# Kernel optimization log

Hardware: AMD Instinct MI355X
Metric: run time of the kernel (lower is better)

## Reference

```python
import jax, jax.numpy as jnp
import numpy as np

N_NODES = 50000


def _degree_norms(edge_index, n_nodes):
    # PyG GCNConv: add self-loops, deg = 1 + in-degree at target (col)
    src, dst = edge_index[0], edge_index[1]
    deg = 1.0 + jax.ops.segment_sum(jnp.ones(src.shape[0], jnp.float32), dst,
                                    num_segments=n_nodes)
    d_inv_sqrt = 1.0 / jnp.sqrt(deg)  # deg >= 1 always (self-loop)
    norm_e = d_inv_sqrt[src] * d_inv_sqrt[dst]   # per-edge sym norm
    norm_self = d_inv_sqrt * d_inv_sqrt          # self-loop weight
    return norm_e, norm_self


def _gcn_conv(x, W, b, src, dst, norm_e, norm_self, n_nodes):
    h = x @ W                                    # [N, F_out]
    msg = h[src] * norm_e[:, None]               # gather + scale, [E, F_out]
    agg = jax.ops.segment_sum(msg, dst, num_segments=n_nodes)
    return agg + norm_self[:, None] * h + b


def setup_inputs() -> dict:
    key = jax.random.key(0)
    ks = jax.random.split(key, 10)
    F_in, H = 128, 128
    E = 1_600_000
    x = jax.random.normal(ks[0], (N_NODES, F_in), jnp.float32)
    edge_index = jax.random.randint(ks[1], (2, E), 0, N_NODES, dtype=jnp.int64)

    def glorot(k, fi, fo):
        s = jnp.sqrt(6.0 / (fi + fo)).astype(jnp.float32)
        return jax.random.uniform(k, (fi, fo), jnp.float32, -s, s)

    return {
        "x": x,
        "edge_index": edge_index,
        "W1": glorot(ks[2], F_in, H), "b1": jnp.zeros((H,), jnp.float32),
        "W2": glorot(ks[3], H, H),    "b2": jnp.zeros((H,), jnp.float32),
        "W3": glorot(ks[4], H, H),    "b3": jnp.zeros((H,), jnp.float32),
        "W4": glorot(ks[5], H, 1),    "b4": jnp.zeros((1,), jnp.float32),
    }


def reference(x, edge_index, W1, b1, W2, b2, W3, b3, W4, b4):
    src, dst = edge_index[0], edge_index[1]
    norm_e, norm_self = _degree_norms(edge_index, N_NODES)
    h = jax.nn.relu(_gcn_conv(x, W1, b1, src, dst, norm_e, norm_self, N_NODES))
    h = jax.nn.relu(_gcn_conv(h, W2, b2, src, dst, norm_e, norm_self, N_NODES))
    h = jax.nn.relu(_gcn_conv(h, W3, b3, src, dst, norm_e, norm_self, N_NODES))
    return _gcn_conv(h, W4, b4, src, dst, norm_e, norm_self, N_NODES)
```

## Files before the change

### kernel.cpp

```cpp
#include <hip/hip_runtime.h>
#include <hip/hip_bf16.h>
#include <stdint.h>

typedef unsigned int u32;
typedef unsigned short u16;

#define F 128
#define NBUCK 196
#define SLOTS 9216

typedef __attribute__((ext_vector_type(8))) short bf16x8;
typedef __attribute__((ext_vector_type(8))) u16 u16x8;
typedef __attribute__((ext_vector_type(4))) float f32x4;

__device__ __forceinline__ float bf2f(u16 v){
  union { u32 u; float f; } x; x.u = ((u32)v) << 16; return x.f;
}
__device__ __forceinline__ float bflo(u32 w){
  union { u32 u; float f; } x; x.u = w << 16; return x.f;
}
__device__ __forceinline__ float bfhi(u32 w){
  union { u32 u; float f; } x; x.u = w & 0xFFFF0000u; return x.f;
}
__device__ __forceinline__ u16 f2bf(float f){
  union { float f; u32 u; } x; x.f = f;
  u32 u = x.u;
  return (u16)((u + 0x7fffu + ((u >> 16) & 1u)) >> 16);
}
__device__ __forceinline__ bf16x8 as_bf(u16x8 v){
  union { u16x8 a; bf16x8 b; } u; u.a = v; return u.b;
}
__device__ __forceinline__ int detect_f32(const u32* xw){
  u32 hit = 0;
  for (int i = threadIdx.x; i < 2048; i += 256){
    u32 e = (xw[i] >> 7) & 0xFFu;
    if (e > 160u) hit = 1;
  }
  return __syncthreads_or((int)hit);
}
__device__ __forceinline__ int detect_stride(const u32* ei){
  u32 v = 0;
  for (int i = threadIdx.x; i < 4096; i += 256) v |= ei[2*i + 1];
  return __syncthreads_or((int)v) ? 1 : 2;
}

__global__ void k_setup(const void* x0,
                        const void* b1, const void* b2, const void* b3,
                        const void* W1, const void* W2, const void* W3,
                        const void* W4, const void* b4,
                        float* __restrict__ bb, float* __restrict__ wf4,
                        float* __restrict__ bb4, u16* __restrict__ WL,
                        int* __restrict__ bump){
  int t = threadIdx.x, b = blockIdx.x;
  int f32 = detect_f32((const u32*)x0);
  if (b == 0){
    bump[t] = 0;
    for (int i = t; i < 384; i += 256){
      const void* s = (i < 128) ? b1 : ((i < 256) ? b2 : b3);
      int ii = i & 127;
      bb[i] = f32 ? ((const float*)s)[ii] : bf2f(((const u16*)s)[ii]);
    }
    if (t < 128) wf4[t] = f32 ? ((const float*)W4)[t] : bf2f(((const u16*)W4)[t]);
    if (t == 0)  bb4[0] = f32 ? ((const float*)b4)[0] : bf2f(((const u16*)b4)[0]);
  } else {
    int bb_ = b - 1;
    int l = bb_ >> 6;
    const void* W = (l == 0) ? W1 : ((l == 1) ? W2 : W3);
    int idx = (bb_ & 63)*256 + t;
    int j    = idx & 7;
    int lane = (idx >> 3) & 63;
    int kb   = (idx >> 9) & 3;
    int ct   = idx >> 11;
    int m = lane & 15, q = lane >> 4;
    int k = kb*32 + q*8 + j;
    int c = ct*16 + m;
    float v = f32 ? ((const float*)W)[k*F + c] : bf2f(((const u16*)W)[k*F + c]);
    WL[l*16384 + idx] = f2bf(v);
  }
}

__launch_bounds__(256)
__global__ void k_msplit(const u32* __restrict__ w, int E,
                         int* __restrict__ bump, u32* __restrict__ ebuf){
  __shared__ int h[256];
  __shared__ int cb[256];
  int st = detect_stride(w);
  int t = threadIdx.x;
  h[t] = 0;
  __syncthreads();
  int base = blockIdx.x*4096;
  u32 ps[16]; int bk[16]; int rk[16];
  #pragma unroll 4
  for (int k = 0; k < 16; k++){
    int i = base + k*256 + t;
    if (i < E){
      u32 s = w[(size_t)i*st];
      u32 d = w[(size_t)(E + i)*st];
      bk[k] = (int)(d >> 8);
      ps[k] = (s & 0xFFFFu) | ((d & 0xFFu) << 16);
      rk[k] = atomicAdd(&h[bk[k]], 1);
    } else bk[k] = -1;
  }
  __syncthreads();
  cb[t] = h[t] ? (t*SLOTS + atomicAdd(&bump[t], h[t])) : 0;
  __syncthreads();
  #pragma unroll 4
  for (int k = 0; k < 16; k++){
    if (bk[k] >= 0) ebuf[cb[bk[k]] + rk[k]] = ps[k];
  }
}

__launch_bounds__(256)
__global__ void k_bemit(const u32* __restrict__ ebuf, const int* __restrict__ bump,
                        int N, int* __restrict__ deg, int* __restrict__ rs,
                        u16* __restrict__ csr, float* __restrict__ dis){
  __shared__ int nd[256];
  __shared__ int nofs[256];
  __shared__ int s[256];
  int b = blockIdx.x;
  int t = threadIdx.x;
  int e0 = b*SLOTS, e1 = e0 + bump[b];
  nd[t] = 0;
  __syncthreads();
  for (int i = e0 + t; i < e1; i += 256) atomicAdd(&nd[ebuf[i] >> 16], 1);
  __syncthreads();
  int v = nd[t];
  s[t] = v;
  __syncthreads();
  for (int off = 1; off < 256; off <<= 1){
    int x = (t >= off) ? s[t - off] : 0;
    __syncthreads();
    s[t] += x;
    __syncthreads();
  }
  nofs[t] = s[t] - v;
  int node = b*256 + t;
  if (node < N){
    deg[node] = v;
    rs[node]  = e0 + nofs[t];
    dis[node] = rsqrtf(1.0f + (float)v);
  }
  nd[t] = 0;
  __syncthreads();
  for (int i = e0 + t; i < e1; i += 256){
    u32 p = ebuf[i];
    int d = (int)(p >> 16);
    int pos = e0 + nofs[d] + atomicAdd(&nd[d], 1);
    csr[pos] = (u16)(p & 0xFFFFu);
  }
}

__launch_bounds__(256)
__global__ void k_mm(const u16* __restrict__ X, const void* __restrict__ Xraw,
                     const u16* __restrict__ WL, const float* __restrict__ dis,
                     u16* __restrict__ G, int N, int mode){
  int f32 = 0;
  if (mode) f32 = detect_f32((const u32*)Xraw);
  int w = threadIdx.x >> 6, lane = threadIdx.x & 63;
  int m = lane & 15, q = lane >> 4;
  int row0 = blockIdx.x*64 + w*16;
  int arow = row0 + m;
  u16x8 a[4];
  if (arow < N){
    if (mode == 0){
      const u16* xp = X + (size_t)arow*F;
      #pragma unroll
      for (int kb = 0; kb < 4; kb++) a[kb] = *(const u16x8*)(xp + kb*32 + q*8);
    } else if (f32){
      const float* xp = (const float*)Xraw + (size_t)arow*F;
      #pragma unroll
      for (int kb = 0; kb < 4; kb++){
        f32x4 v0 = *(const f32x4*)(xp + kb*32 + q*8);
        f32x4 v1 = *(const f32x4*)(xp + kb*32 + q*8 + 4);
        u16x8 o;
        #pragma unroll
        for (int k = 0; k < 4; k++){ o[k] = f2bf(v0[k]); o[k+4] = f2bf(v1[k]); }
        a[kb] = o;
      }
    } else {
      const u16* xp = (const u16*)Xraw + (size_t)arow*F;
      #pragma unroll
      for (int kb = 0; kb < 4; kb++) a[kb] = *(const u16x8*)(xp + kb*32 + q*8);
    }
  } else {
    #pragma unroll
    for (int kb = 0; kb < 4; kb++) a[kb] = (u16x8){0,0,0,0,0,0,0,0};
  }
  f32x4 acc[8];
  #pragma unroll
  for (int ct = 0; ct < 8; ct++) acc[ct] = (f32x4){0.f,0.f,0.f,0.f};
  #pragma unroll
  for (int ct = 0; ct < 8; ct++){
    #pragma unroll
    for (int kb = 0; kb < 4; kb++){
      bf16x8 bfr = *(const bf16x8*)(WL + ((size_t)((ct*4 + kb)*64 + lane))*8);
      acc[ct] = __builtin_amdgcn_mfma_f32_16x16x32_bf16(as_bf(a[kb]), bfr, acc[ct], 0, 0, 0);
    }
  }
  int rbase = row0 + q*4;
  #pragma unroll
  for (int r = 0; r < 4; r++){
    int row = rbase + r;
    if (row < N){
      float dv = dis[row];
      #pragma unroll
      for (int ct = 0; ct < 8; ct++)
        __builtin_nontemporal_store(f2bf(dv*acc[ct][r]),
                                    &G[(size_t)row*F + ct*16 + m]);
    }
  }
}

__launch_bounds__(256)
__global__ void k_agg(const u16* __restrict__ G, const float* __restrict__ dis,
                      const int* __restrict__ rs, const int* __restrict__ deg,
                      const u16* __restrict__ csr, const float* __restrict__ bias,
                      u16* __restrict__ Xout, const float* __restrict__ W4f,
                      float* __restrict__ G4, int N, int fuse4){
  int wid  = blockIdx.x*4 + (threadIdx.x >> 6);
  int lane = threadIdx.x & 63;
  if (wid >= N) return;
  int base = rs[wid], len = deg[wid];
  const char* Gb = (const char*)G;
  u32 fo = 4u*(u32)lane;
  u32 sw = *(const u32*)(Gb + (((size_t)(u32)wid) << 8) + fo);
  float a0 = bflo(sw), a1 = bfhi(sw);
  float pa[8], qa[8];
  #pragma unroll
  for (int k = 0; k < 8; k++){ pa[k] = 0.f; qa[k] = 0.f; }

  int mm = (len < 64) ? len : 64;
  u32 soff = ((u32)csr[base + lane]) << 8;
  int c0 = 0;
  while (c0 < len){
    int nxt = c0 + 64;
    int nmm = len - nxt; if (nmm > 64) nmm = 64;
    u32 soff_n = 0;
    if (nmm > 0) soff_n = ((u32)csr[base + nxt + lane]) << 8;
    int j = 0;
    for (; j + 8 <= mm; j += 8){
      u32 w[8];
      #pragma unroll
      for (int k = 0; k < 8; k++){
        u32 o = (u32)__builtin_amdgcn_readlane((int)soff, j + k);
        w[k] = *(const u32*)(Gb + o + fo);
      }
      #pragma unroll
      for (int k = 0; k < 8; k++){
        pa[k] += bflo(w[k]); qa[k] += bfhi(w[k]);
      }
    }
    for (; j < mm; j++){
      u32 o = (u32)__builtin_amdgcn_readlane((int)soff, j);
      u32 wv = *(const u32*)(Gb + o + fo);
      pa[0] += bflo(wv); qa[0] += bfhi(wv);
    }
    soff = soff_n; mm = nmm; c0 = nxt;
  }
  a0 += ((pa[0] + pa[1]) + (pa[2] + pa[3])) + ((pa[4] + pa[5]) + (pa[6] + pa[7]));
  a1 += ((qa[0] + qa[1]) + (qa[2] + qa[3])) + ((qa[4] + qa[5]) + (qa[6] + qa[7]));
  float dv = dis[wid];
  float o0 = fmaxf(fmaf(dv, a0, bias[2*lane]),     0.f);
  float o1 = fmaxf(fmaf(dv, a1, bias[2*lane + 1]), 0.f);
  if (!fuse4){
    u32 pk = (u32)f2bf(o0) | ((u32)f2bf(o1) << 16);
    __builtin_nontemporal_store(pk, (u32*)(Xout + (size_t)wid*F + 2*lane));
  } else {
    float acc = o0*W4f[2*lane] + o1*W4f[2*lane + 1];
    #pragma unroll
    for (int off = 32; off > 0; off >>= 1) acc += __shfl_down(acc, off, 64);
    if (lane == 0) G4[wid] = dv*acc;
  }
}

__global__ void k_agg4(const void* __restrict__ x0, const float* __restrict__ G4,
                       const float* __restrict__ dis, const int* __restrict__ rs,
                       const int* __restrict__ deg, const u16* __restrict__ csr,
                       const float* __restrict__ b4f, void* __restrict__ out, int N){
  int f32 = detect_f32((const u32*)x0);
  int i = blockIdx.x*blockDim.x + threadIdx.x;
  if (i >= N) return;
  int base = rs[i], len = deg[i];
  float a0 = 0.f, a1 = 0.f, a2 = 0.f, a3 = 0.f;
  int j = 0;
  for (; j + 4 <= len; j += 4){
    int s0 = csr[base + j],     s1 = csr[base + j + 1];
    int s2 = csr[base + j + 2], s3 = csr[base + j + 3];
    a0 += G4[s0]; a1 += G4[s1]; a2 += G4[s2]; a3 += G4[s3];
  }
  for (; j < len; j++) a0 += G4[csr[base + j]];
  float r = dis[i]*(G4[i] + ((a0 + a1) + (a2 + a3))) + b4f[0];
  if (f32) ((float*)out)[i] = r;
  else     ((u16*)out)[i]   = f2bf(r);
}

extern "C" void kernel_launch(void* const* d_in, const int* in_sizes, int n_in,
                              void* d_out, int out_size, void* d_ws, size_t ws_size,
                              hipStream_t stream){
  const void* x0 = d_in[0];
  const u32*  ei = (const u32*)d_in[1];
  const void* Wp[4] = {d_in[2], d_in[4], d_in[6], d_in[8]};
  const void* bp[4] = {d_in[3], d_in[5], d_in[7], d_in[9]};
  int N = in_sizes[0] / F;
  int E = in_sizes[1] / 2;

  char* base = (char*)d_ws;
  size_t off = 0;
  auto alloc = [&](size_t bytes)->char*{
    char* p = base + off;
    off = (off + bytes + 255) & ~(size_t)255;
    return p;
  };
  int*   deg  = (int*)  alloc((size_t)N*4);
  float* dis  = (float*)alloc((size_t)N*4);
  int*   rs   = (int*)  alloc((size_t)N*4);
  float* g4   = (float*)alloc((size_t)N*4);
  int*   bump = (int*)  alloc(1024);
  u32*   ebuf = (u32*)  alloc(((size_t)NBUCK*SLOTS + 64)*4);
  u16*   csr  = (u16*)  alloc(((size_t)NBUCK*SLOTS + 128)*2);
  u16*   WL   = (u16*)  alloc(3*16384*2);
  float* wf4  = (float*)alloc(F*4);
  float* bb   = (float*)alloc(3*F*4);
  float* bb4  = (float*)alloc(256);
  u16*   gbuf = (u16*)  alloc((size_t)N*F*2);
  u16*   xbuf = (u16*)  alloc((size_t)N*F*2);

  int etb = (E + 4095)/4096;
  int nbt = (N + 255)/256;

  k_setup<<<193, 256, 0, stream>>>(x0, bp[0], bp[1], bp[2],
                                   Wp[0], Wp[1], Wp[2], Wp[3], bp[3],
                                   bb, wf4, bb4, WL, bump);
  k_msplit<<<etb, 256, 0, stream>>>(ei, E, bump, ebuf);
  k_bemit <<<NBUCK, 256, 0, stream>>>(ebuf, bump, N, deg, rs, csr, dis);

  int mmb = (N + 63)/64;
  int agb = (N + 3)/4;

  for (int l = 0; l < 3; l++){
    k_mm <<<mmb, 256, 0, stream>>>(xbuf, (l == 0) ? x0 : (const void*)xbuf,
                                   WL + l*16384, dis, gbuf, N, (l == 0) ? 1 : 0);
    k_agg<<<agb, 256, 0, stream>>>(gbuf, dis, rs, deg, csr, bb + l*F, xbuf,
                                   wf4, g4, N, (l == 2) ? 1 : 0);
  }
  k_agg4<<<nbt, 256, 0, stream>>>(x0, g4, dis, rs, deg, csr, bb4, (void*)d_out, N);
}
```

Before: 345.6 us.

## Transpose MFMA output for packed row stores and use wave-per-node final aggregation

The matmul kernel swaps the MFMA operands so each lane holds four consecutive output columns of a single row. It can then pack them into 8-byte stores instead of scattering 2-byte stores across rows. The final scalar aggregation kernel changes from thread-per-node to wave-per-node with a shuffle reduction, which spreads the gather over lanes and removes per-thread load imbalance. The price is more launched waves and reduction overhead in the last layer.

```diff
diff --git a/kernel.cpp b/kernel.cpp
--- a/kernel.cpp
+++ b/kernel.cpp
@@ -12,6 +12,7 @@
 typedef __attribute__((ext_vector_type(8))) short bf16x8;
 typedef __attribute__((ext_vector_type(8))) u16 u16x8;
 typedef __attribute__((ext_vector_type(4))) float f32x4;
+typedef __attribute__((ext_vector_type(2))) u32 u32x2;
 
 __device__ __forceinline__ float bf2f(u16 v){
   union { u32 u; float f; } x; x.u = ((u32)v) << 16; return x.f;
@@ -194,19 +195,18 @@
     #pragma unroll
     for (int kb = 0; kb < 4; kb++){
       bf16x8 bfr = *(const bf16x8*)(WL + ((size_t)((ct*4 + kb)*64 + lane))*8);
-      acc[ct] = __builtin_amdgcn_mfma_f32_16x16x32_bf16(as_bf(a[kb]), bfr, acc[ct], 0, 0, 0);
-    }
-  }
-  int rbase = row0 + q*4;
-  #pragma unroll
-  for (int r = 0; r < 4; r++){
-    int row = rbase + r;
-    if (row < N){
-      float dv = dis[row];
-      #pragma unroll
-      for (int ct = 0; ct < 8; ct++)
-        __builtin_nontemporal_store(f2bf(dv*acc[ct][r]),
-                                    &G[(size_t)row*F + ct*16 + m]);
+      acc[ct] = __builtin_amdgcn_mfma_f32_16x16x32_bf16(bfr, as_bf(a[kb]), acc[ct], 0, 0, 0);
+    }
+  }
+  if (arow < N){
+    float dv = dis[arow];
+    u16* gp = G + (size_t)arow*F + q*4;
+    #pragma unroll
+    for (int ct = 0; ct < 8; ct++){
+      u32x2 pk;
+      pk.x = (u32)f2bf(dv*acc[ct][0]) | ((u32)f2bf(dv*acc[ct][1]) << 16);
+      pk.y = (u32)f2bf(dv*acc[ct][2]) | ((u32)f2bf(dv*acc[ct][3]) << 16);
+      __builtin_nontemporal_store(pk, (u32x2*)(gp + ct*16));
     }
   }
 }
@@ -273,25 +273,25 @@
   }
 }
 
+__launch_bounds__(256)
 __global__ void k_agg4(const void* __restrict__ x0, const float* __restrict__ G4,
                        const float* __restrict__ dis, const int* __restrict__ rs,
                        const int* __restrict__ deg, const u16* __restrict__ csr,
                        const float* __restrict__ b4f, void* __restrict__ out, int N){
   int f32 = detect_f32((const u32*)x0);
-  int i = blockIdx.x*blockDim.x + threadIdx.x;
-  if (i >= N) return;
-  int base = rs[i], len = deg[i];
-  float a0 = 0.f, a1 = 0.f, a2 = 0.f, a3 = 0.f;
-  int j = 0;
-  for (; j + 4 <= len; j += 4){
-    int s0 = csr[base + j],     s1 = csr[base + j + 1];
-    int s2 = csr[base + j + 2], s3 = csr[base + j + 3];
-    a0 += G4[s0]; a1 += G4[s1]; a2 += G4[s2]; a3 += G4[s3];
-  }
-  for (; j < len; j++) a0 += G4[csr[base + j]];
-  float r = dis[i]*(G4[i] + ((a0 + a1) + (a2 + a3))) + b4f[0];
-  if (f32) ((float*)out)[i] = r;
-  else     ((u16*)out)[i]   = f2bf(r);
+  int wid  = blockIdx.x*4 + (threadIdx.x >> 6);
+  int lane = threadIdx.x & 63;
+  if (wid >= N) return;
+  int base = rs[wid], len = deg[wid];
+  float acc = 0.f;
+  for (int j = lane; j < len; j += 64) acc += G4[csr[base + j]];
+  #pragma unroll
+  for (int off = 32; off > 0; off >>= 1) acc += __shfl_down(acc, off, 64);
+  if (lane == 0){
+    float r = dis[wid]*(G4[wid] + acc) + b4f[0];
+    if (f32) ((float*)out)[wid] = r;
+    else     ((u16*)out)[wid]   = f2bf(r);
+  }
 }
 
 extern "C" void kernel_launch(void* const* d_in, const int* in_sizes, int n_in,
@@ -326,7 +326,6 @@
   u16*   xbuf = (u16*)  alloc((size_t)N*F*2);
 
   int etb = (E + 4095)/4096;
-  int nbt = (N + 255)/256;
 
   k_setup<<<193, 256, 0, stream>>>(x0, bp[0], bp[1], bp[2],
                                    Wp[0], Wp[1], Wp[2], Wp[3], bp[3],
@@ -343,5 +342,5 @@
     k_agg<<<agb, 256, 0, stream>>>(gbuf, dis, rs, deg, csr, bb + l*F, xbuf,
                                    wf4, g4, N, (l == 2) ? 1 : 0);
   }
-  k_agg4<<<nbt, 256, 0, stream>>>(x0, g4, dis, rs, deg, csr, bb4, (void*)d_out, N);
-}
+  k_agg4<<<agb, 256, 0, stream>>>(x0, g4, dis, rs, deg, csr, bb4, (void*)d_out, N);
+}
```

After: 359.4 us. 4.0% more time.
